# Kernel tuning notes

Measured on AMD Instinct MI355X. Metric: run time of the kernel, lower is better.

The kernel has to match this reference:

```python
import jax, jax.numpy as jnp
import numpy as np

B, T, IN = 16, 2048, 65
WIN = 12            # win_length
CTX = 2 * WIN + 1   # 25-frame window
HID = 64
LAYERS = 3


def setup_inputs() -> dict:
    key = jax.random.key(0)
    ks = jax.random.split(key, 2 + 4 * LAYERS + 2)
    d = {"input_audio": jax.random.normal(ks[0], (B, T, IN), jnp.float32)}
    in_dims = [IN * CTX, HID, HID]
    s = 1.0 / np.sqrt(HID)
    k = 1
    for l in range(LAYERS):
        d[f"Wih{l}"] = jax.random.uniform(ks[k], (4 * HID, in_dims[l]), jnp.float32, -s, s); k += 1
        d[f"Whh{l}"] = jax.random.uniform(ks[k], (4 * HID, HID), jnp.float32, -s, s); k += 1
        d[f"bih{l}"] = jax.random.uniform(ks[k], (4 * HID,), jnp.float32, -s, s); k += 1
        d[f"bhh{l}"] = jax.random.uniform(ks[k], (4 * HID,), jnp.float32, -s, s); k += 1
    d["Wout"] = jax.random.uniform(ks[k], (1, HID), jnp.float32, -s, s); k += 1
    d["bout"] = jax.random.uniform(ks[k], (1,), jnp.float32, -s, s)
    return d


def concate_frames(x):
    # x: [B, T, D] -> [B, T, CTX*D] via zero-padded sliding window (single gather)
    pad = jnp.pad(x, ((0, 0), (WIN, WIN), (0, 0)))
    idx = jnp.arange(x.shape[1])[:, None] + jnp.arange(CTX)[None, :]  # [T, CTX]
    win = pad[:, idx]                                                 # [B, T, CTX, D]
    return win.reshape(x.shape[0], x.shape[1], CTX * x.shape[2])


def lstm_layer(x, Wih, Whh, bih, bhh):
    # x: [B, T, Din] -> [B, T, HID]; PyTorch gate order i, f, g, o
    pre = jnp.einsum('btd,gd->btg', x, Wih) + bih + bhh  # [B, T, 4H]
    h0 = jnp.zeros((x.shape[0], HID), x.dtype)

    def step(carry, p_t):
        h, c = carry
        g = p_t + h @ Whh.T
        i, f, gg, o = jnp.split(g, 4, axis=-1)
        c = jax.nn.sigmoid(f) * c + jax.nn.sigmoid(i) * jnp.tanh(gg)
        h = jax.nn.sigmoid(o) * jnp.tanh(c)
        return (h, c), h

    _, hs = jax.lax.scan(step, (h0, h0), jnp.swapaxes(pre, 0, 1))
    return jnp.swapaxes(hs, 0, 1)


def reference(input_audio, Wih0, Whh0, bih0, bhh0, Wih1, Whh1, bih1, bhh1,
              Wih2, Whh2, bih2, bhh2, Wout, bout):
    x = concate_frames(input_audio)
    x = lstm_layer(x, Wih0, Whh0, bih0, bhh0)
    x = lstm_layer(x, Wih1, Whh1, bih1, bhh1)
    x = lstm_layer(x, Wih2, Whh2, bih2, bhh2)
    x = jax.nn.relu(x)
    x = jnp.einsum('bth,oh->bto', x, Wout) + bout  # [B, T, 1]
    return jax.nn.sigmoid(x[:, :, 0])
```

## Files before the change

### kernel.cpp

```cpp
#include <hip/hip_runtime.h>
#include <stdint.h>

#define GLOBAL_AS __attribute__((address_space(1)))
#define LDS_AS    __attribute__((address_space(3)))

typedef _Float16 f16;
typedef _Float16 half8 __attribute__((ext_vector_type(8)));
typedef float    f32x4 __attribute__((ext_vector_type(4)));

constexpr int B_  = 16;
constexpr int T_  = 2048;
constexpr int IN_ = 65;
constexpr int HID = 64;
constexpr int G4  = 256;
constexpr int FW  = 72;
constexpr int KP  = 1824;
constexpr int KC0 = KP / 32;

constexpr size_t OFF_XF   = 0;
constexpr size_t SZ_XF    = (size_t)B_ * T_ * FW * 2;
constexpr size_t OFF_WP0  = OFF_XF + SZ_XF;
constexpr size_t SZ_WP0   = (size_t)KC0 * 16 * 64 * 8 * 2;
constexpr size_t OFF_WHHF = OFF_WP0 + SZ_WP0;
constexpr size_t SZ_WHHF1 = (size_t)16 * 2 * 64 * 8 * 2;
constexpr size_t OFF_WIHR = OFF_WHHF + 3 * SZ_WHHF1;
constexpr size_t SZ_WIHR1 = (size_t)16 * 2 * 64 * 8 * 2;
constexpr size_t OFF_BC   = OFF_WIHR + 2 * SZ_WIHR1;
constexpr size_t OFF_PRE  = ((OFF_BC + 3 * 256 * 4 + 1023) / 1024) * 1024;
constexpr size_t SZ_PRE   = (size_t)T_ * B_ * G4 * 4;
constexpr size_t OFF_H2   = OFF_PRE + SZ_PRE;
constexpr size_t SZ_H     = (size_t)B_ * T_ * HID * 2;

__device__ __forceinline__ void async_copy16(const void* g, void* l) {
  __builtin_amdgcn_global_load_lds((const GLOBAL_AS void*)g, (LDS_AS void*)l, 16, 0, 0);
}

__device__ __forceinline__ int pre_col_byte(int g) {
  int j = g & 63, q = g >> 6;
  return (j << 4) | (q << 2);
}

__device__ __forceinline__ float fsig(float x) {
  return __builtin_amdgcn_rcpf(1.f + __builtin_amdgcn_exp2f(-1.4426950408889634f * x));
}
__device__ __forceinline__ float ftanh(float x) {
  return 1.f - 2.f * __builtin_amdgcn_rcpf(1.f + __builtin_amdgcn_exp2f(2.8853900817779268f * x));
}

__global__ void pack_kernel(const float* __restrict__ in0, const float* __restrict__ Wih0,
                            const float* __restrict__ Whh0, const float* __restrict__ bih0, const float* __restrict__ bhh0,
                            const float* __restrict__ Wih1, const float* __restrict__ Whh1, const float* __restrict__ bih1, const float* __restrict__ bhh1,
                            const float* __restrict__ Wih2, const float* __restrict__ Whh2, const float* __restrict__ bih2, const float* __restrict__ bhh2,
                            f16* __restrict__ xf, f16* __restrict__ wp0,
                            f16* __restrict__ whhf, f16* __restrict__ wihr, float* __restrict__ bc)
{
  const int stride = gridDim.x * blockDim.x;
  const int tid0 = blockIdx.x * blockDim.x + threadIdx.x;

  const int NX = B_ * T_ * FW;
  for (int i = tid0; i < NX; i += stride) {
    int f = i % FW; int bt = i / FW;
    float v = (f < IN_) ? in0[(size_t)bt * IN_ + f] : 0.f;
    xf[i] = (f16)v;
  }
  const int NW0 = KC0 * 16 * 64 * 8;
  for (int i = tid0; i < NW0; i += stride) {
    int j = i & 7, l = (i >> 3) & 63, nt = (i >> 9) & 15, kc = i >> 13;
    int kp = kc * 32 + ((l >> 4) * 8 + j);
    int g  = nt * 16 + (l & 15);
    int d = kp / FW, f = kp % FW;
    float v = (kp < 1800 && f < IN_) ? Wih0[(size_t)g * 1625 + d * IN_ + f] : 0.f;
    wp0[i] = (f16)v;
  }
  const float* whhs[3] = {Whh0, Whh1, Whh2};
  for (int i = tid0; i < 3 * 16384; i += stride) {
    int L = i >> 14, r = i & 16383;
    int e = r & 7, l = (r >> 3) & 63, kf = (r >> 9) & 1, tt = (r >> 10) & 15;
    int wv = tt >> 2, u = tt & 3;
    int g = u * 64 + wv * 16 + (l & 15);
    int k = kf * 32 + ((l >> 4) * 8) + e;
    whhf[i] = (f16)whhs[L][g * 64 + k];
  }
  const float* wihs[2] = {Wih1, Wih2};
  for (int i = tid0; i < 2 * 16384; i += stride) {
    int L = i >> 14, r = i & 16383;
    int e = r & 7, l = (r >> 3) & 63, kf = (r >> 9) & 1, tt = (r >> 10) & 15;
    int wv = tt >> 2, u = tt & 3;
    int g = u * 64 + wv * 16 + (l & 15);
    int k = kf * 32 + ((l >> 4) * 8) + e;
    wihr[i] = (f16)wihs[L][g * 64 + k];
  }
  const float* bis[3] = {bih0, bih1, bih2};
  const float* bhs[3] = {bhh0, bhh1, bhh2};
  for (int i = tid0; i < 3 * 256; i += stride) {
    int L = i >> 8, g = i & 255;
    bc[i] = bis[L][g] + bhs[L][g];
  }
}

__global__ __launch_bounds__(256) void gemm0_kernel(const f16* __restrict__ xf, const f16* __restrict__ wp0,
                                                    const float* __restrict__ bc0, float* __restrict__ pre)
{
  __shared__ __align__(16) f16 frames[90 * FW];
  __shared__ __align__(16) f16 bbuf[16 * 64 * 8];
  const int tid = threadIdx.x, l = tid & 63, w = tid >> 6;
  const int b = blockIdx.y, t0 = blockIdx.x * 64;

  for (int c = tid; c < 810; c += 256) *(f32x4*)(&frames[c * 8]) = (f32x4)0.f;
  __syncthreads();

  {
    const int st = t0 - 12;
    const int s0 = st < 0 ? 0 : st;
    const int s1 = (t0 + 78) < T_ ? (t0 + 78) : T_;
    const int dstrow = s0 - st;
    const int nchunk = (s1 - s0) * 9;
    const f16* gsrc = xf + ((size_t)b * T_ + s0) * FW;
    for (int base = 0; base < 810; base += 256) {
      int idx = base + w * 64 + l;
      if (idx < nchunk) {
        char* ldsb = (char*)frames + dstrow * 144 + (base + w * 64) * 16;
        async_copy16((const char*)gsrc + (size_t)(base + w * 64) * 16 + l * 16, ldsb);
      }
    }
  }

  f32x4 acc[16];
#pragma unroll
  for (int i = 0; i < 16; ++i) acc[i] = (f32x4)0.f;

  for (int kc = 0; kc < KC0; ++kc) {
    __syncthreads();
    const f16* wsrc = wp0 + (size_t)kc * 8192;
#pragma unroll
    for (int i = 0; i < 4; ++i) {
      char* ldsb = (char*)bbuf + (i * 256 + w * 64) * 16;
      async_copy16((const char*)wsrc + (size_t)(i * 256 + w * 64 + l) * 16, ldsb);
    }
    __syncthreads();

    int kp0 = kc * 32 + ((l >> 4) * 8);
    int d = kp0 / FW, f = kp0 % FW;
    int r = w * 16 + (l & 15);
    half8 af = *(const half8*)(&frames[(r + d) * FW + f]);
#pragma unroll
    for (int nt = 0; nt < 16; ++nt) {
      half8 bf = *(const half8*)(&bbuf[(nt * 64 + l) * 8]);
      acc[nt] = __builtin_amdgcn_mfma_f32_16x16x32_f16(af, bf, acc[nt], 0, 0, 0);
    }
  }

  const int n_ = l & 15, grp = l >> 4;
#pragma unroll
  for (int nt = 0; nt < 16; ++nt) {
    int g = nt * 16 + n_;
    float bias = bc0[g];
    int colByte = pre_col_byte(g);
#pragma unroll
    for (int rr = 0; rr < 4; ++rr) {
      int t = t0 + w * 16 + grp * 4 + rr;
      *(float*)((char*)pre + (size_t)t * 16384 + (size_t)b * 1024 + colByte) = acc[nt][rr] + bias;
    }
  }
}

__global__ __launch_bounds__(768) void r3_kernel(const float* __restrict__ pre,
                                                 const f16* __restrict__ whhf,
                                                 const f16* __restrict__ wihr,
                                                 const float* __restrict__ bc,
                                                 f16* __restrict__ h2out)
{
  __shared__ __align__(16) char hring[6 * 640];
  const int tid = threadIdx.x, l = tid & 63, w = tid >> 6;
  const int L = w >> 2, wv = w & 3;
  const int n_ = l & 15, grp = l >> 4;
  const int b0 = blockIdx.x * 4;
  const int j = wv * 16 + n_;
  const int bglob = b0 + grp;
  const int arow = n_ >> 2;

  half8 bfh[4][2];
  const f16* wh = whhf + (size_t)L * 16384;
#pragma unroll
  for (int u = 0; u < 4; ++u)
#pragma unroll
    for (int kf = 0; kf < 2; ++kf)
      bfh[u][kf] = *(const half8*)(wh + (((wv * 4 + u) * 2 + kf) << 9) + (l << 3));

  half8 bfx[4][2];
  if (L > 0) {
    const f16* wx = wihr + (size_t)(L - 1) * 16384;
#pragma unroll
    for (int u = 0; u < 4; ++u)
#pragma unroll
      for (int kf = 0; kf < 2; ++kf)
        bfx[u][kf] = *(const half8*)(wx + (((wv * 4 + u) * 2 + kf) << 9) + (l << 3));
  }

  float bi[4] = {0.f, 0.f, 0.f, 0.f};
  if (L > 0) {
#pragma unroll
    for (int u = 0; u < 4; ++u) bi[u] = bc[L * 256 + u * 64 + j];
  }

  for (int i = tid; i < 240; i += 768) *(f32x4*)(hring + i * 16) = (f32x4)0.f;
  float c = 0.f;

  const int lp = L & 1;
  const int Lm1 = (L > 0) ? (L - 1) : 0;
  const char* ownRd0 = hring + (L * 2 + (1 ^ lp)) * 640 + arow * 160 + grp * 16;
  const char* ownRd1 = hring + (L * 2 + (0 ^ lp)) * 640 + arow * 160 + grp * 16;
  const char* inRd0  = hring + (Lm1 * 2 + (0 ^ lp)) * 640 + arow * 160 + grp * 16;
  const char* inRd1  = hring + (Lm1 * 2 + (1 ^ lp)) * 640 + arow * 160 + grp * 16;
  char* wr0 = hring + (L * 2 + (0 ^ lp)) * 640 + grp * 160 + j * 2;
  char* wr1 = hring + (L * 2 + (1 ^ lp)) * 640 + grp * 160 + j * 2;

  f32x4 P0 = (f32x4)0.f, P1 = (f32x4)0.f, P2 = (f32x4)0.f, P3 = (f32x4)0.f;
  const GLOBAL_AS char* preP =
      (const GLOBAL_AS char*)(uintptr_t)((const char*)pre + (size_t)bglob * 1024 + (size_t)j * 16);
  if (L == 0) {
    P0 = *(const GLOBAL_AS f32x4*)(preP);
    P1 = *(const GLOBAL_AS f32x4*)(preP + 16384);
    P2 = *(const GLOBAL_AS f32x4*)(preP + 32768);
    preP += 3 * 16384;
  }
  GLOBAL_AS f16* h2p = (GLOBAL_AS f16*)(uintptr_t)(h2out + (size_t)bglob * T_ * HID + j);

#define R3STEP(S_, PU_, PLD_, SP_)                                              \
  {                                                                             \
    asm volatile("s_waitcnt lgkmcnt(0)" ::: "memory");                          \
    __builtin_amdgcn_s_barrier();                                               \
    __builtin_amdgcn_sched_barrier(0);                                          \
    const int t = (S_) - L;                                                     \
    const bool act = (unsigned)t < (unsigned)T_;                                \
    if (L == 0 && (t + 3) < T_) {                                               \
      PLD_ = *(const GLOBAL_AS f32x4*)(preP);                                   \
      preP += 16384;                                                            \
    }                                                                           \
    if (act) {                                                                  \
      const char* Hc = (SP_) ? ownRd1 : ownRd0;                                 \
      half8 a0 = *(const half8*)(Hc);                                           \
      half8 a1 = *(const half8*)(Hc + 64);                                      \
      f32x4 acc[4];                                                             \
      _Pragma("unroll")                                                         \
      for (int u = 0; u < 4; ++u) {                                             \
        acc[u] = __builtin_amdgcn_mfma_f32_16x16x32_f16(a0, bfh[u][0], (f32x4)0.f, 0, 0, 0); \
        acc[u] = __builtin_amdgcn_mfma_f32_16x16x32_f16(a1, bfh[u][1], acc[u], 0, 0, 0);     \
      }                                                                         \
      if (L > 0) {                                                              \
        const char* Xc = (SP_) ? inRd1 : inRd0;                                 \
        half8 x0 = *(const half8*)(Xc);                                         \
        half8 x1 = *(const half8*)(Xc + 64);                                    \
        _Pragma("unroll")                                                       \
        for (int u = 0; u < 4; ++u) {                                           \
          acc[u] = __builtin_amdgcn_mfma_f32_16x16x32_f16(x0, bfx[u][0], acc[u], 0, 0, 0);   \
          acc[u] = __builtin_amdgcn_mfma_f32_16x16x32_f16(x1, bfx[u][1], acc[u], 0, 0, 0);   \
        }                                                                       \
      }                                                                         \
      float iv, fv, gv, ov;                                                     \
      if (L == 0) {                                                             \
        iv = acc[0][0] + PU_.x; fv = acc[1][0] + PU_.y;                         \
        gv = acc[2][0] + PU_.z; ov = acc[3][0] + PU_.w;                         \
      } else {                                                                  \
        iv = acc[0][0] + bi[0]; fv = acc[1][0] + bi[1];                         \
        gv = acc[2][0] + bi[2]; ov = acc[3][0] + bi[3];                         \
      }                                                                         \
      c = fsig(fv) * c + fsig(iv) * ftanh(gv);                                  \
      float hv = fsig(ov) * ftanh(c);                                           \
      f16 h16 = (f16)hv;                                                        \
      *(f16*)((SP_) ? wr1 : wr0) = h16;                                         \
      if (L == 2) { *h2p = h16; h2p += HID; }                                   \
    }                                                                           \
  }

  for (int s4 = 0; s4 < T_ + 4; s4 += 4) {
    R3STEP(s4 + 0, P0, P3, 0)
    R3STEP(s4 + 1, P1, P0, 1)
    R3STEP(s4 + 2, P2, P1, 0)
    R3STEP(s4 + 3, P3, P2, 1)
  }
#undef R3STEP
}

__global__ __launch_bounds__(256) void fin_kernel(const f16* __restrict__ h2, const float* __restrict__ Wout,
                                                  const float* __restrict__ bout, float* __restrict__ out)
{
  __shared__ float wl[64];
  const int tid = threadIdx.x;
  if (tid < 64) wl[tid] = Wout[tid];
  __syncthreads();
  const int idx = blockIdx.x * 256 + tid;
  const f16* hr = h2 + (size_t)idx * HID;
  float acc = bout[0];
#pragma unroll
  for (int i = 0; i < 64; i += 8) {
    half8 hv = *(const half8*)(hr + i);
#pragma unroll
    for (int k = 0; k < 8; ++k) {
      float h = (float)hv[k];
      h = fmaxf(h, 0.f);
      acc += h * wl[i + k];
    }
  }
  out[idx] = fsig(acc);
}

extern "C" void kernel_launch(void* const* d_in, const int* in_sizes, int n_in,
                              void* d_out, int out_size, void* d_ws, size_t ws_size,
                              hipStream_t stream)
{
  (void)in_sizes; (void)n_in; (void)out_size; (void)ws_size;
  const float* in0  = (const float*)d_in[0];
  const float* Wih0 = (const float*)d_in[1];
  const float* Whh0 = (const float*)d_in[2];
  const float* bih0 = (const float*)d_in[3];
  const float* bhh0 = (const float*)d_in[4];
  const float* Wih1 = (const float*)d_in[5];
  const float* Whh1 = (const float*)d_in[6];
  const float* bih1 = (const float*)d_in[7];
  const float* bhh1 = (const float*)d_in[8];
  const float* Wih2 = (const float*)d_in[9];
  const float* Whh2 = (const float*)d_in[10];
  const float* bih2 = (const float*)d_in[11];
  const float* bhh2 = (const float*)d_in[12];
  const float* Wout = (const float*)d_in[13];
  const float* bout = (const float*)d_in[14];
  float* out = (float*)d_out;

  char* ws = (char*)d_ws;
  f16*   xf   = (f16*)(ws + OFF_XF);
  f16*   wp0  = (f16*)(ws + OFF_WP0);
  f16*   whhf = (f16*)(ws + OFF_WHHF);
  f16*   wihr = (f16*)(ws + OFF_WIHR);
  float* bc   = (float*)(ws + OFF_BC);
  float* pre  = (float*)(ws + OFF_PRE);
  f16*   h2   = (f16*)(ws + OFF_H2);

  pack_kernel<<<256, 256, 0, stream>>>(in0, Wih0, Whh0, bih0, bhh0,
                                       Wih1, Whh1, bih1, bhh1,
                                       Wih2, Whh2, bih2, bhh2,
                                       xf, wp0, whhf, wihr, bc);
  gemm0_kernel<<<dim3(32, 16), 256, 0, stream>>>(xf, wp0, bc, pre);
  r3_kernel<<<4, 768, 0, stream>>>(pre, whhf, wihr, bc, h2);
  fin_kernel<<<128, 256, 0, stream>>>(h2, Wout, bout, out);
}
```

Baseline: 1.427 ms.

## Split recurrent LSTM kernel into 8 blocks of 2 batches with 2 waves per layer

```diff
diff --git a/kernel.cpp b/kernel.cpp
--- a/kernel.cpp
+++ b/kernel.cpp
@@ -76,8 +76,8 @@
   for (int i = tid0; i < 3 * 16384; i += stride) {
     int L = i >> 14, r = i & 16383;
     int e = r & 7, l = (r >> 3) & 63, kf = (r >> 9) & 1, tt = (r >> 10) & 15;
-    int wv = tt >> 2, u = tt & 3;
-    int g = u * 64 + wv * 16 + (l & 15);
+    int jb = tt >> 2, u = tt & 3;
+    int g = u * 64 + jb * 16 + (l & 15);
     int k = kf * 32 + ((l >> 4) * 8) + e;
     whhf[i] = (f16)whhs[L][g * 64 + k];
   }
@@ -85,8 +85,8 @@
   for (int i = tid0; i < 2 * 16384; i += stride) {
     int L = i >> 14, r = i & 16383;
     int e = r & 7, l = (r >> 3) & 63, kf = (r >> 9) & 1, tt = (r >> 10) & 15;
-    int wv = tt >> 2, u = tt & 3;
-    int g = u * 64 + wv * 16 + (l & 15);
+    int jb = tt >> 2, u = tt & 3;
+    int g = u * 64 + jb * 16 + (l & 15);
     int k = kf * 32 + ((l >> 4) * 8) + e;
     wihr[i] = (f16)wihs[L][g * 64 + k];
   }
@@ -164,37 +164,47 @@
   }
 }
 
-__global__ __launch_bounds__(768) void r3_kernel(const float* __restrict__ pre,
-                                                 const f16* __restrict__ whhf,
-                                                 const f16* __restrict__ wihr,
-                                                 const float* __restrict__ bc,
-                                                 f16* __restrict__ h2out)
-{
-  __shared__ __align__(16) char hring[6 * 640];
+__global__ __launch_bounds__(384, 2) void r6_kernel(const float* __restrict__ pre,
+                                                    const f16* __restrict__ whhf,
+                                                    const f16* __restrict__ wihr,
+                                                    const float* __restrict__ bc,
+                                                    f16* __restrict__ h2out)
+{
+  __shared__ __align__(16) char hring[6 * 256];
   const int tid = threadIdx.x, l = tid & 63, w = tid >> 6;
-  const int L = w >> 2, wv = w & 3;
+  const int L = w >> 1, wv = w & 1;
   const int n_ = l & 15, grp = l >> 4;
-  const int b0 = blockIdx.x * 4;
-  const int j = wv * 16 + n_;
-  const int bglob = b0 + grp;
-  const int arow = n_ >> 2;
-
-  half8 bfh[4][2];
+  const int jb_own = wv * 2 + (grp & 1);
+  const int j  = jb_own * 16 + n_;
+  const int b_loc = grp >> 1;
+  const int bglob = blockIdx.x * 2 + b_loc;
+  const int arow = n_ >> 3;
+  const bool selB = (grp & 1) != 0;
+
+  half8 bfh[2][4][2];
   const f16* wh = whhf + (size_t)L * 16384;
 #pragma unroll
-  for (int u = 0; u < 4; ++u)
-#pragma unroll
-    for (int kf = 0; kf < 2; ++kf)
-      bfh[u][kf] = *(const half8*)(wh + (((wv * 4 + u) * 2 + kf) << 9) + (l << 3));
-
-  half8 bfx[4][2];
+  for (int ji = 0; ji < 2; ++ji)
+#pragma unroll
+    for (int u = 0; u < 4; ++u)
+#pragma unroll
+      for (int kf = 0; kf < 2; ++kf) {
+        int tt = (wv * 2 + ji) * 4 + u;
+        bfh[ji][u][kf] = *(const half8*)(wh + (((tt * 2) + kf) << 9) + (l << 3));
+      }
+
+  half8 bfx[2][4][2];
   if (L > 0) {
     const f16* wx = wihr + (size_t)(L - 1) * 16384;
 #pragma unroll
-    for (int u = 0; u < 4; ++u)
-#pragma unroll
-      for (int kf = 0; kf < 2; ++kf)
-        bfx[u][kf] = *(const half8*)(wx + (((wv * 4 + u) * 2 + kf) << 9) + (l << 3));
+    for (int ji = 0; ji < 2; ++ji)
+#pragma unroll
+      for (int u = 0; u < 4; ++u)
+#pragma unroll
+        for (int kf = 0; kf < 2; ++kf) {
+          int tt = (wv * 2 + ji) * 4 + u;
+          bfx[ji][u][kf] = *(const half8*)(wx + (((tt * 2) + kf) << 9) + (l << 3));
+        }
   }
 
   float bi[4] = {0.f, 0.f, 0.f, 0.f};
@@ -203,17 +213,17 @@
     for (int u = 0; u < 4; ++u) bi[u] = bc[L * 256 + u * 64 + j];
   }
 
-  for (int i = tid; i < 240; i += 768) *(f32x4*)(hring + i * 16) = (f32x4)0.f;
+  if (tid < 96) *(f32x4*)(hring + tid * 16) = (f32x4)0.f;
   float c = 0.f;
 
   const int lp = L & 1;
   const int Lm1 = (L > 0) ? (L - 1) : 0;
-  const char* ownRd0 = hring + (L * 2 + (1 ^ lp)) * 640 + arow * 160 + grp * 16;
-  const char* ownRd1 = hring + (L * 2 + (0 ^ lp)) * 640 + arow * 160 + grp * 16;
-  const char* inRd0  = hring + (Lm1 * 2 + (0 ^ lp)) * 640 + arow * 160 + grp * 16;
-  const char* inRd1  = hring + (Lm1 * 2 + (1 ^ lp)) * 640 + arow * 160 + grp * 16;
-  char* wr0 = hring + (L * 2 + (0 ^ lp)) * 640 + grp * 160 + j * 2;
-  char* wr1 = hring + (L * 2 + (1 ^ lp)) * 640 + grp * 160 + j * 2;
+  const char* ownRd0 = hring + (L * 2 + (1 ^ lp)) * 256 + arow * 128 + grp * 16;
+  const char* ownRd1 = hring + (L * 2 + (0 ^ lp)) * 256 + arow * 128 + grp * 16;
+  const char* inRd0  = hring + (Lm1 * 2 + (0 ^ lp)) * 256 + arow * 128 + grp * 16;
+  const char* inRd1  = hring + (Lm1 * 2 + (1 ^ lp)) * 256 + arow * 128 + grp * 16;
+  char* wr0 = hring + (L * 2 + (0 ^ lp)) * 256 + b_loc * 128 + j * 2;
+  char* wr1 = hring + (L * 2 + (1 ^ lp)) * 256 + b_loc * 128 + j * 2;
 
   f32x4 P0 = (f32x4)0.f, P1 = (f32x4)0.f, P2 = (f32x4)0.f, P3 = (f32x4)0.f;
   const GLOBAL_AS char* preP =
@@ -226,60 +236,71 @@
   }
   GLOBAL_AS f16* h2p = (GLOBAL_AS f16*)(uintptr_t)(h2out + (size_t)bglob * T_ * HID + j);
 
-#define R3STEP(S_, PU_, PLD_, SP_)                                              \
-  {                                                                             \
-    asm volatile("s_waitcnt lgkmcnt(0)" ::: "memory");                          \
-    __builtin_amdgcn_s_barrier();                                               \
-    __builtin_amdgcn_sched_barrier(0);                                          \
-    const int t = (S_) - L;                                                     \
-    const bool act = (unsigned)t < (unsigned)T_;                                \
-    if (L == 0 && (t + 3) < T_) {                                               \
-      PLD_ = *(const GLOBAL_AS f32x4*)(preP);                                   \
-      preP += 16384;                                                            \
-    }                                                                           \
-    if (act) {                                                                  \
-      const char* Hc = (SP_) ? ownRd1 : ownRd0;                                 \
-      half8 a0 = *(const half8*)(Hc);                                           \
-      half8 a1 = *(const half8*)(Hc + 64);                                      \
-      f32x4 acc[4];                                                             \
-      _Pragma("unroll")                                                         \
-      for (int u = 0; u < 4; ++u) {                                             \
-        acc[u] = __builtin_amdgcn_mfma_f32_16x16x32_f16(a0, bfh[u][0], (f32x4)0.f, 0, 0, 0); \
-        acc[u] = __builtin_amdgcn_mfma_f32_16x16x32_f16(a1, bfh[u][1], acc[u], 0, 0, 0);     \
-      }                                                                         \
-      if (L > 0) {                                                              \
-        const char* Xc = (SP_) ? inRd1 : inRd0;                                 \
-        half8 x0 = *(const half8*)(Xc);                                         \
-        half8 x1 = *(const half8*)(Xc + 64);                                    \
-        _Pragma("unroll")                                                       \
-        for (int u = 0; u < 4; ++u) {                                           \
-          acc[u] = __builtin_amdgcn_mfma_f32_16x16x32_f16(x0, bfx[u][0], acc[u], 0, 0, 0);   \
-          acc[u] = __builtin_amdgcn_mfma_f32_16x16x32_f16(x1, bfx[u][1], acc[u], 0, 0, 0);   \
-        }                                                                       \
-      }                                                                         \
-      float iv, fv, gv, ov;                                                     \
-      if (L == 0) {                                                             \
-        iv = acc[0][0] + PU_.x; fv = acc[1][0] + PU_.y;                         \
-        gv = acc[2][0] + PU_.z; ov = acc[3][0] + PU_.w;                         \
-      } else {                                                                  \
-        iv = acc[0][0] + bi[0]; fv = acc[1][0] + bi[1];                         \
-        gv = acc[2][0] + bi[2]; ov = acc[3][0] + bi[3];                         \
-      }                                                                         \
-      c = fsig(fv) * c + fsig(iv) * ftanh(gv);                                  \
-      float hv = fsig(ov) * ftanh(c);                                           \
-      f16 h16 = (f16)hv;                                                        \
-      *(f16*)((SP_) ? wr1 : wr0) = h16;                                         \
-      if (L == 2) { *h2p = h16; h2p += HID; }                                   \
-    }                                                                           \
+#define R6STEP(S_, PU_, PLD_, SP_)                                                             \
+  {                                                                                            \
+    asm volatile("s_waitcnt lgkmcnt(0)" ::: "memory");                                         \
+    __builtin_amdgcn_s_barrier();                                                              \
+    __builtin_amdgcn_sched_barrier(0);                                                         \
+    const int t = (S_) - L;                                                                    \
+    const bool act = (unsigned)t < (unsigned)T_;                                               \
+    if (L == 0 && (t + 3) < T_) {                                                              \
+      PLD_ = *(const GLOBAL_AS f32x4*)(preP);                                                  \
+      preP += 16384;                                                                           \
+    }                                                                                          \
+    if (act) {                                                                                 \
+      const char* Hc = (SP_) ? ownRd1 : ownRd0;                                                \
+      half8 a0 = *(const half8*)(Hc);                                                          \
+      half8 a1 = *(const half8*)(Hc + 64);                                                     \
+      f32x4 aA[4], aB[4];                                                                      \
+      if (L > 0) {                                                                             \
+        const char* Xc = (SP_) ? inRd1 : inRd0;                                                \
+        half8 x0 = *(const half8*)(Xc);                                                        \
+        half8 x1 = *(const half8*)(Xc + 64);                                                   \
+        _Pragma("unroll")                                                                      \
+        for (int u = 0; u < 4; ++u) {                                                          \
+          aA[u] = __builtin_amdgcn_mfma_f32_16x16x32_f16(x0, bfx[0][u][0], (f32x4)0.f, 0, 0, 0); \
+          aA[u] = __builtin_amdgcn_mfma_f32_16x16x32_f16(x1, bfx[0][u][1], aA[u], 0, 0, 0);    \
+          aA[u] = __builtin_amdgcn_mfma_f32_16x16x32_f16(a0, bfh[0][u][0], aA[u], 0, 0, 0);    \
+          aA[u] = __builtin_amdgcn_mfma_f32_16x16x32_f16(a1, bfh[0][u][1], aA[u], 0, 0, 0);    \
+          aB[u] = __builtin_amdgcn_mfma_f32_16x16x32_f16(x0, bfx[1][u][0], (f32x4)0.f, 0, 0, 0); \
+          aB[u] = __builtin_amdgcn_mfma_f32_16x16x32_f16(x1, bfx[1][u][1], aB[u], 0, 0, 0);    \
+          aB[u] = __builtin_amdgcn_mfma_f32_16x16x32_f16(a0, bfh[1][u][0], aB[u], 0, 0, 0);    \
+          aB[u] = __builtin_amdgcn_mfma_f32_16x16x32_f16(a1, bfh[1][u][1], aB[u], 0, 0, 0);    \
+        }                                                                                      \
+      } else {                                                                                 \
+        _Pragma("unroll")                                                                      \
+        for (int u = 0; u < 4; ++u) {                                                          \
+          aA[u] = __builtin_amdgcn_mfma_f32_16x16x32_f16(a0, bfh[0][u][0], (f32x4)0.f, 0, 0, 0); \
+          aA[u] = __builtin_amdgcn_mfma_f32_16x16x32_f16(a1, bfh[0][u][1], aA[u], 0, 0, 0);    \
+          aB[u] = __builtin_amdgcn_mfma_f32_16x16x32_f16(a0, bfh[1][u][0], (f32x4)0.f, 0, 0, 0); \
+          aB[u] = __builtin_amdgcn_mfma_f32_16x16x32_f16(a1, bfh[1][u][1], aB[u], 0, 0, 0);    \
+        }                                                                                      \
+      }                                                                                        \
+      float g0 = selB ? aB[0][0] : aA[0][0];                                                   \
+      float g1 = selB ? aB[1][0] : aA[1][0];                                                   \
+      float g2 = selB ? aB[2][0] : aA[2][0];                                                   \
+      float g3 = selB ? aB[3][0] : aA[3][0];                                                   \
+      float iv, fv, gv, ov;                                                                    \
+      if (L == 0) {                                                                            \
+        iv = g0 + PU_.x; fv = g1 + PU_.y; gv = g2 + PU_.z; ov = g3 + PU_.w;                    \
+      } else {                                                                                 \
+        iv = g0 + bi[0]; fv = g1 + bi[1]; gv = g2 + bi[2]; ov = g3 + bi[3];                    \
+      }                                                                                        \
+      c = fsig(fv) * c + fsig(iv) * ftanh(gv);                                                 \
+      float hv = fsig(ov) * ftanh(c);                                                          \
+      f16 h16v = (f16)hv;                                                                      \
+      *(f16*)((SP_) ? wr1 : wr0) = h16v;                                                       \
+      if (L == 2) { *h2p = h16v; h2p += HID; }                                                 \
+    }                                                                                          \
   }
 
   for (int s4 = 0; s4 < T_ + 4; s4 += 4) {
-    R3STEP(s4 + 0, P0, P3, 0)
-    R3STEP(s4 + 1, P1, P0, 1)
-    R3STEP(s4 + 2, P2, P1, 0)
-    R3STEP(s4 + 3, P3, P2, 1)
-  }
-#undef R3STEP
+    R6STEP(s4 + 0, P0, P3, 0)
+    R6STEP(s4 + 1, P1, P0, 1)
+    R6STEP(s4 + 2, P2, P1, 0)
+    R6STEP(s4 + 3, P3, P2, 1)
+  }
+#undef R6STEP
 }
 
 __global__ __launch_bounds__(256) void fin_kernel(const f16* __restrict__ h2, const float* __restrict__ Wout,
@@ -341,6 +362,6 @@
                                        Wih2, Whh2, bih2, bhh2,
                                        xf, wp0, whhf, wihr, bc);
   gemm0_kernel<<<dim3(32, 16), 256, 0, stream>>>(xf, wp0, bc, pre);
-  r3_kernel<<<4, 768, 0, stream>>>(pre, whhf, wihr, bc, h2);
+  r6_kernel<<<8, 384, 0, stream>>>(pre, whhf, wihr, bc, h2);
   fin_kernel<<<128, 256, 0, stream>>>(h2, Wout, bout, out);
 }
```

After: 1.323 ms. -7.3%, faster.
